# Optimization experiments

Hardware: AMD Instinct MI355X
Metric: run time of the kernel (lower is better)

## Reference

```python
import jax, jax.numpy as jnp
import numpy as np

INF = 1.0e12
B, L, D, H = 8, 128, 512, 8
DV = D // H

def _xavier(key, shape, fan_in, fan_out):
    a = float(np.sqrt(6.0 / (fan_in + fan_out)))
    return jax.random.uniform(key, shape, jnp.float32, -a, a)

def setup_inputs() -> dict:
    key = jax.random.key(0)
    ks = jax.random.split(key, 12)
    inp = jax.random.normal(ks[0], (B, L, D), jnp.float32)
    relation_inp = jax.random.normal(ks[1], (B, L, L, D), jnp.float32)
    mask = jnp.zeros((B, L, L), dtype=bool)  # no padding masked
    adj_mask = jax.random.randint(ks[2], (B, H, L, L), 0, 2).astype(jnp.int32)
    idx = jnp.arange(L)
    adj_mask = adj_mask.at[:, :, idx, idx].set(1)  # ensure non-empty neighborhoods
    rel_pos_mat = jnp.zeros((B, L, L), jnp.int32)
    deprel_mat = jnp.zeros((B, L, L), jnp.int32)
    deparc_mat = jnp.zeros((B, L, L), jnp.int32)
    W_value = _xavier(ks[3], (D, H * DV), D, H * DV)
    W_relation = _xavier(ks[4], (D, H * DV), D, H * DV)
    # weight vectors have torch shape (1,1,1,H,DV); xavier fan over last 2 dims
    w_src = _xavier(ks[5], (H, DV), H, DV)
    w_tgt = _xavier(ks[6], (H, DV), H, DV)
    w_rel = _xavier(ks[7], (H, DV), H, DV)
    W_final = _xavier(ks[8], (2 * D, D), 2 * D, D)
    b_final = jnp.zeros((D,), jnp.float32)
    return {"inp": inp, "relation_inp": relation_inp, "mask": mask,
            "adj_mask": adj_mask, "rel_pos_mat": rel_pos_mat,
            "deprel_mat": deprel_mat, "deparc_mat": deparc_mat,
            "W_value": W_value, "W_relation": W_relation,
            "w_src": w_src, "w_tgt": w_tgt, "w_rel": w_rel,
            "W_final": W_final, "b_final": b_final}

def _leaky(x):
    return jnp.where(x >= 0, x, 0.2 * x)

def reference(inp, relation_inp, mask, adj_mask, rel_pos_mat, deprel_mat,
              deparc_mat, W_value, W_relation, w_src, w_tgt, w_rel,
              W_final, b_final):
    b, l, d = inp.shape
    h, dv = w_src.shape
    # value: [B,H,L,DV]
    value = (inp @ W_value).reshape(b, l, h, dv).transpose(0, 2, 1, 3)
    # additive GAT scores without materializing [B,L,L,H,DV] src/tgt tensors
    e_src = jnp.einsum('bhld,hd->bhl', value, w_src)  # source index j
    e_tgt = jnp.einsum('bhld,hd->bhl', value, w_tgt)  # target index i
    scores_value = _leaky(e_tgt[:, :, :, None] + e_src[:, :, None, :])  # [B,H,L,L]
    # relation projection: [B,L,L,H,DV]
    relation = (relation_inp @ W_relation).reshape(b, l, l, h, dv)
    scores_relation = _leaky(jnp.einsum('bijhd,hd->bhij', relation, w_rel))
    # masks
    pad = mask[:, None]                       # [B,1,L,L] True = masked
    noadj = adj_mask == 0                     # [B,H,L,L]
    bad = pad | noadj
    scores_value = jnp.where(bad, -INF, scores_value)
    scores_relation = jnp.where(bad, -INF, scores_relation)
    attn_value = jax.nn.softmax(scores_value, axis=-1)
    attn_relation = jax.nn.softmax(scores_relation, axis=-1)
    # normalized: multiply by 1/adj (0 where no edge since adj in {0,1}), L1 renorm
    adjf = adj_mask.astype(attn_value.dtype)
    def renorm(a):
        a = a * adjf
        s = jnp.sum(jnp.abs(a), axis=-1, keepdims=True)
        return a / jnp.maximum(s, 1e-12)
    attn_value = renorm(attn_value)
    attn_relation = renorm(attn_relation)
    # zero masked / non-adjacent entries
    attn_value = jnp.where(bad, 0.0, attn_value)
    attn_relation = jnp.where(bad, 0.0, attn_relation)
    out_v = jnp.einsum('bhij,bhjd->bhid', attn_value, value)
    out_r = jnp.einsum('bhij,bhjd->bhid', attn_relation, value)
    out_v = out_v.transpose(0, 2, 1, 3).reshape(b, l, h * dv)
    out_r = out_r.transpose(0, 2, 1, 3).reshape(b, l, h * dv)
    final = jnp.concatenate([out_v, out_r], axis=-1) @ W_final + b_final
    final = final + inp
    return final, attn_value, attn_relation
```

## Files before the change

### kernel.cpp

```cpp
#include <hip/hip_runtime.h>

#define B_ 8
#define L_ 128
#define D_ 512
#define H_ 8

__device__ __forceinline__ float leaky(float v) { return fmaxf(v, 0.2f * v); }

__global__ __launch_bounds__(256) void k_value_wreff(
        const float* __restrict__ inp, const float* __restrict__ Wv,
        const float* __restrict__ wsrc, const float* __restrict__ wtgt,
        const float* __restrict__ Wrel, const float* __restrict__ wrel,
        float* __restrict__ value_t, float* __restrict__ e_src,
        float* __restrict__ e_tgt, float* __restrict__ wr_eff) {
    __shared__ float xs[4][512];
    const int t = threadIdx.x;

    if (blockIdx.x >= 256) {
        int g = (blockIdx.x - 256) * 256 + t;
        int k = g >> 3, h = g & 7;
        const float4* a = (const float4*)(Wrel + k * 512 + h * 64);
        const float4* b = (const float4*)(wrel + h * 64);
        float acc = 0.f;
#pragma unroll
        for (int q = 0; q < 16; q++) {
            float4 av = a[q], bv = b[q];
            acc += av.x * bv.x + av.y * bv.y + av.z * bv.z + av.w * bv.w;
        }
        wr_eff[k * 8 + h] = acc;
        return;
    }

    const int row0 = blockIdx.x * 4;
    {
        int r = t >> 6, seg = t & 63;
        const float4* ip = (const float4*)(inp + (size_t)(row0 + r) * 512 + seg * 8);
        float4 a = ip[0], bq = ip[1];
        *(float4*)&xs[r][seg * 8]     = a;
        *(float4*)&xs[r][seg * 8 + 4] = bq;
    }
    __syncthreads();
    const int c0 = t * 2;
    float acc[4][2] = {};
    for (int k0 = 0; k0 < 512; k0 += 4) {
        float4 xr[4];
#pragma unroll
        for (int r = 0; r < 4; r++) xr[r] = *(const float4*)&xs[r][k0];
#define VSTEP(COMP, I)                                                          \
        {                                                                       \
            float2 wv = *(const float2*)(Wv + (size_t)(k0 + I) * 512 + c0);     \
            _Pragma("unroll")                                                   \
            for (int r = 0; r < 4; r++) {                                       \
                acc[r][0] = fmaf(xr[r].COMP, wv.x, acc[r][0]);                  \
                acc[r][1] = fmaf(xr[r].COMP, wv.y, acc[r][1]);                  \
            }                                                                   \
        }
        VSTEP(x, 0) VSTEP(y, 1) VSTEP(z, 2) VSTEP(w, 3)
#undef VSTEP
    }
    const int h = t >> 5;
    const int d0 = c0 & 63;
    const int b = row0 >> 7, l0 = row0 & 127;
    {
        float4 v0 = make_float4(acc[0][0], acc[1][0], acc[2][0], acc[3][0]);
        float4 v1 = make_float4(acc[0][1], acc[1][1], acc[2][1], acc[3][1]);
        *(float4*)&value_t[((size_t)((b * 8 + h) * 64 + d0)) * 128 + l0] = v0;
        *(float4*)&value_t[((size_t)((b * 8 + h) * 64 + d0 + 1)) * 128 + l0] = v1;
    }
    float ws0 = wsrc[c0], ws1 = wsrc[c0 + 1];
    float wt0 = wtgt[c0], wt1 = wtgt[c0 + 1];
    float es[4], et[4];
#pragma unroll
    for (int r = 0; r < 4; r++) {
        es[r] = acc[r][0] * ws0 + acc[r][1] * ws1;
        et[r] = acc[r][0] * wt0 + acc[r][1] * wt1;
    }
#pragma unroll
    for (int off = 16; off >= 1; off >>= 1)
#pragma unroll
        for (int r = 0; r < 4; r++) {
            es[r] += __shfl_xor(es[r], off, 64);
            et[r] += __shfl_xor(et[r], off, 64);
        }
    if ((t & 31) == 0) {
#pragma unroll
        for (int r = 0; r < 4; r++) {
            e_src[(b * 8 + h) * 128 + l0 + r] = es[r];
            e_tgt[(b * 8 + h) * 128 + l0 + r] = et[r];
        }
    }
}

__global__ __launch_bounds__(256) void k_srel(const float* __restrict__ rel,
                                              const float* __restrict__ wr_eff,
                                              float* __restrict__ s_rel) {
    const int lane = threadIdx.x & 63;
    const int wave = (blockIdx.x * 256 + threadIdx.x) >> 6;

    float wrl[64];
    {
        const float4* wp = (const float4*)(wr_eff + lane * 64);
#pragma unroll
        for (int q = 0; q < 16; q++) {
            float4 v = wp[q];
            wrl[q * 4 + 0] = v.x; wrl[q * 4 + 1] = v.y;
            wrl[q * 4 + 2] = v.z; wrl[q * 4 + 3] = v.w;
        }
    }

    const bool hi32 = (lane & 32) != 0;
    const bool hi16 = (lane & 16) != 0;
    const bool hi8  = (lane & 8) != 0;
    const int  hsel = (lane >> 3) & 7;

#pragma unroll 2
    for (int it = 0; it < 16; ++it) {
        int row = wave + it * 8192;
        const float4* rp = (const float4*)(rel + (size_t)row * 512 + lane * 8);
        float4 u0 = rp[0];
        float4 u1 = rp[1];
        float x[8];
        x[0] = u0.x; x[1] = u0.y; x[2] = u0.z; x[3] = u0.w;
        x[4] = u1.x; x[5] = u1.y; x[6] = u1.z; x[7] = u1.w;
        float acc[8] = {0.f,0.f,0.f,0.f,0.f,0.f,0.f,0.f};
#pragma unroll
        for (int kk = 0; kk < 8; kk++)
#pragma unroll
            for (int h = 0; h < 8; h++)
                acc[h] = fmaf(x[kk], wrl[kk * 8 + h], acc[h]);

        float a4[4];
#pragma unroll
        for (int hh = 0; hh < 4; hh++) {
            float send = hi32 ? acc[hh] : acc[hh + 4];
            float recv = __shfl_xor(send, 32, 64);
            float own  = hi32 ? acc[hh + 4] : acc[hh];
            a4[hh] = own + recv;
        }
        float a2[2];
#pragma unroll
        for (int hh = 0; hh < 2; hh++) {
            float send = hi16 ? a4[hh] : a4[hh + 2];
            float recv = __shfl_xor(send, 16, 64);
            float own  = hi16 ? a4[hh + 2] : a4[hh];
            a2[hh] = own + recv;
        }
        float send = hi8 ? a2[0] : a2[1];
        float recv = __shfl_xor(send, 8, 64);
        float a1 = (hi8 ? a2[1] : a2[0]) + recv;
        a1 += __shfl_xor(a1, 4, 64);
        a1 += __shfl_xor(a1, 2, 64);
        a1 += __shfl_xor(a1, 1, 64);

        if ((lane & 7) == 0) {
            float v = leaky(a1);
            int b = row >> 14, rem = row & 16383;
            s_rel[(((size_t)(b * 8 + hsel)) << 14) + rem] = v;
        }
    }
}

__global__ __launch_bounds__(256) void k_attn(const float* s_rel,
                                              const float* __restrict__ value_t,
                                              const float* __restrict__ e_src,
                                              const float* __restrict__ e_tgt,
                                              const int* __restrict__ adj,
                                              const unsigned char* __restrict__ mask,
                                              float* __restrict__ X,
                                              float* __restrict__ out_av,
                                              float* out_ar) {
    __shared__ float lav[4][128];
    __shared__ float lar[4][128];
    const int t = threadIdx.x;
    const int bh = blockIdx.x >> 5;
    const int iq = blockIdx.x & 31;
    const int b = bh >> 3;

    const int lane = t & 63;
    const int w = t >> 6;
    const int i = iq * 4 + w;
    const size_t rowbase = ((size_t)bh * 128 + i) * 128;
    const float etg = e_tgt[bh * 128 + i];
    const int j0 = lane, j1 = lane + 64;

    float sv0 = leaky(etg + e_src[bh * 128 + j0]);
    float sv1 = leaky(etg + e_src[bh * 128 + j1]);
    float sr0 = s_rel[rowbase + j0];
    float sr1 = s_rel[rowbase + j1];
    int a0 = adj[rowbase + j0], a1 = adj[rowbase + j1];
    unsigned char m0 = mask[(size_t)(b * 128 + i) * 128 + j0];
    unsigned char m1 = mask[(size_t)(b * 128 + i) * 128 + j1];
    bool bad0 = m0 || (a0 == 0);
    bool bad1 = m1 || (a1 == 0);
    if (bad0) { sv0 = -1e30f; sr0 = -1e30f; }
    if (bad1) { sv1 = -1e30f; sr1 = -1e30f; }

    float mv = fmaxf(sv0, sv1), mr = fmaxf(sr0, sr1);
#pragma unroll
    for (int off = 32; off >= 1; off >>= 1) {
        mv = fmaxf(mv, __shfl_xor(mv, off, 64));
        mr = fmaxf(mr, __shfl_xor(mr, off, 64));
    }
    float pv0 = bad0 ? 0.f : __expf(sv0 - mv);
    float pv1 = bad1 ? 0.f : __expf(sv1 - mv);
    float pr0 = bad0 ? 0.f : __expf(sr0 - mr);
    float pr1 = bad1 ? 0.f : __expf(sr1 - mr);
    float sumv = pv0 + pv1, sumr = pr0 + pr1;
#pragma unroll
    for (int off = 32; off >= 1; off >>= 1) {
        sumv += __shfl_xor(sumv, off, 64);
        sumr += __shfl_xor(sumr, off, 64);
    }
    float iv = 1.f / fmaxf(sumv, 1e-12f);
    float ir = 1.f / fmaxf(sumr, 1e-12f);
    float av0 = pv0 * iv, av1 = pv1 * iv;
    float ar0 = pr0 * ir, ar1 = pr1 * ir;

    out_av[rowbase + j0] = av0;
    out_av[rowbase + j1] = av1;
    out_ar[rowbase + j0] = ar0;
    out_ar[rowbase + j1] = ar1;

    lav[w][j0] = av0; lav[w][j1] = av1;
    lar[w][j0] = ar0; lar[w][j1] = ar1;
    __syncthreads();

    const float4* vrow = (const float4*)(value_t + ((size_t)bh * 64 + lane) * 128);
    float accv = 0.f, accr = 0.f;
#pragma unroll 8
    for (int jb = 0; jb < 32; jb++) {
        float4 v4 = vrow[jb];
        float4 a4 = *(const float4*)&lav[w][jb * 4];
        float4 r4 = *(const float4*)&lar[w][jb * 4];
        accv = fmaf(a4.x, v4.x, accv); accv = fmaf(a4.y, v4.y, accv);
        accv = fmaf(a4.z, v4.z, accv); accv = fmaf(a4.w, v4.w, accv);
        accr = fmaf(r4.x, v4.x, accr); accr = fmaf(r4.y, v4.y, accr);
        accr = fmaf(r4.z, v4.z, accr); accr = fmaf(r4.w, v4.w, accr);
    }
    const int hh = bh & 7;
    size_t xrow = ((size_t)(b * 128 + i)) * 1024;
    X[xrow + hh * 64 + lane] = accv;
    X[xrow + 512 + hh * 64 + lane] = accr;
}

__global__ __launch_bounds__(256) void k_final(const float* __restrict__ X,
                                               const float* __restrict__ Wf,
                                               const float* __restrict__ bias,
                                               const float* __restrict__ inp,
                                               float* __restrict__ outf) {
    __shared__ float xs[4][1024];
    const int t = threadIdx.x;
    const int row0 = blockIdx.x * 4;
    {
        const float4* src = (const float4*)(X + (size_t)row0 * 1024);
        float4* dst = (float4*)xs;
#pragma unroll
        for (int q = 0; q < 4; q++) dst[q * 256 + t] = src[q * 256 + t];
    }
    __syncthreads();
    const int c0 = t * 2;
    float acc[4][2] = {};
    for (int k0 = 0; k0 < 1024; k0 += 4) {
        float4 xr[4];
#pragma unroll
        for (int r = 0; r < 4; r++) xr[r] = *(const float4*)&xs[r][k0];
#define FSTEP(COMP, I)                                                          \
        {                                                                       \
            float2 wv = *(const float2*)(Wf + (size_t)(k0 + I) * 512 + c0);     \
            _Pragma("unroll")                                                   \
            for (int r = 0; r < 4; r++) {                                       \
                acc[r][0] = fmaf(xr[r].COMP, wv.x, acc[r][0]);                  \
                acc[r][1] = fmaf(xr[r].COMP, wv.y, acc[r][1]);                  \
            }                                                                   \
        }
        FSTEP(x, 0) FSTEP(y, 1) FSTEP(z, 2) FSTEP(w, 3)
#undef FSTEP
    }
    float b0 = bias[c0], b1 = bias[c0 + 1];
#pragma unroll
    for (int r = 0; r < 4; r++) {
        size_t ro = (size_t)(row0 + r) * 512;
        float2 iv = *(const float2*)(inp + ro + c0);
        float v0 = acc[r][0] + b0 + iv.x;
        float v1 = acc[r][1] + b1 + iv.y;
        *(float2*)&outf[ro + c0] = make_float2(v0, v1);
    }
}

extern "C" void kernel_launch(void* const* d_in, const int* in_sizes, int n_in,
                              void* d_out, int out_size, void* d_ws, size_t ws_size,
                              hipStream_t stream) {
    const float* inp  = (const float*)d_in[0];
    const float* rel  = (const float*)d_in[1];
    const unsigned char* mask = (const unsigned char*)d_in[2];
    const int*   adj  = (const int*)d_in[3];
    const float* Wv   = (const float*)d_in[7];
    const float* Wr   = (const float*)d_in[8];
    const float* wsrc = (const float*)d_in[9];
    const float* wtgt = (const float*)d_in[10];
    const float* wrel = (const float*)d_in[11];
    const float* Wf   = (const float*)d_in[12];
    const float* bfin = (const float*)d_in[13];

    float* outf   = (float*)d_out;
    float* out_av = outf + (size_t)B_ * L_ * D_;
    float* out_ar = out_av + (size_t)B_ * H_ * L_ * L_;

    char* ws = (char*)d_ws;
    float* wr_eff  = (float*)(ws);
    float* value_t = (float*)(ws + 16384);
    float* e_src   = (float*)(ws + 2113536);
    float* e_tgt   = (float*)(ws + 2146304);
    float* X       = (float*)(ws + 2179072);

    k_value_wreff<<<272, 256, 0, stream>>>(inp, Wv, wsrc, wtgt, Wr, wrel,
                                           value_t, e_src, e_tgt, wr_eff);
    k_srel<<<2048, 256, 0, stream>>>(rel, wr_eff, out_ar);
    k_attn<<<2048, 256, 0, stream>>>(out_ar, value_t, e_src, e_tgt, adj, mask,
                                     X, out_av, out_ar);
    k_final<<<256, 256, 0, stream>>>(X, Wf, bfin, inp, outf);
}
```

Measured before the change: 550.5 us.

## Fuse value projection into s_rel kernel and attention into final projection

Splits the W_rel·w_rel reduction into its own small kernel. The value/e_src/e_tgt projection blocks now run as extra blocks of the relation-score kernel, so that small GEMM overlaps the large streaming pass. The attention kernel now has each block handle four query rows across all eight heads and keep the concatenated head outputs in shared memory. It then applies W_final, bias and residual in place, which removes the X workspace round trip and one launch. In exchange, the attention stage runs with far fewer blocks and loops over heads serially, which reduces parallelism and latency hiding.

```diff
diff --git a/kernel.cpp b/kernel.cpp
--- a/kernel.cpp
+++ b/kernel.cpp
@@ -7,31 +7,100 @@
 
 __device__ __forceinline__ float leaky(float v) { return fmaxf(v, 0.2f * v); }
 
-__global__ __launch_bounds__(256) void k_value_wreff(
+__global__ __launch_bounds__(256) void k_wreff(const float* __restrict__ Wrel,
+                                               const float* __restrict__ wrel,
+                                               float* __restrict__ wr_eff) {
+    int t = blockIdx.x * 256 + threadIdx.x;
+    int k = t >> 3, h = t & 7;
+    const float4* a = (const float4*)(Wrel + k * 512 + h * 64);
+    const float4* b = (const float4*)(wrel + h * 64);
+    float acc = 0.f;
+#pragma unroll
+    for (int q = 0; q < 16; q++) {
+        float4 av = a[q], bv = b[q];
+        acc += av.x * bv.x + av.y * bv.y + av.z * bv.z + av.w * bv.w;
+    }
+    wr_eff[k * 8 + h] = acc;
+}
+
+__global__ __launch_bounds__(256) void k_srel_value(
+        const float* __restrict__ rel, const float* __restrict__ wr_eff,
         const float* __restrict__ inp, const float* __restrict__ Wv,
         const float* __restrict__ wsrc, const float* __restrict__ wtgt,
-        const float* __restrict__ Wrel, const float* __restrict__ wrel,
-        float* __restrict__ value_t, float* __restrict__ e_src,
-        float* __restrict__ e_tgt, float* __restrict__ wr_eff) {
+        float* __restrict__ s_rel, float* __restrict__ value_t,
+        float* __restrict__ e_src, float* __restrict__ e_tgt) {
     __shared__ float xs[4][512];
     const int t = threadIdx.x;
 
-    if (blockIdx.x >= 256) {
-        int g = (blockIdx.x - 256) * 256 + t;
-        int k = g >> 3, h = g & 7;
-        const float4* a = (const float4*)(Wrel + k * 512 + h * 64);
-        const float4* b = (const float4*)(wrel + h * 64);
-        float acc = 0.f;
-#pragma unroll
-        for (int q = 0; q < 16; q++) {
-            float4 av = a[q], bv = b[q];
-            acc += av.x * bv.x + av.y * bv.y + av.z * bv.z + av.w * bv.w;
-        }
-        wr_eff[k * 8 + h] = acc;
+    if (blockIdx.x < 2048) {
+        const int lane = t & 63;
+        const int wave = (blockIdx.x * 256 + t) >> 6;
+
+        float wrl[64];
+        {
+            const float4* wp = (const float4*)(wr_eff + lane * 64);
+#pragma unroll
+            for (int q = 0; q < 16; q++) {
+                float4 v = wp[q];
+                wrl[q * 4 + 0] = v.x; wrl[q * 4 + 1] = v.y;
+                wrl[q * 4 + 2] = v.z; wrl[q * 4 + 3] = v.w;
+            }
+        }
+
+        const bool hi32 = (lane & 32) != 0;
+        const bool hi16 = (lane & 16) != 0;
+        const bool hi8  = (lane & 8) != 0;
+        const int  hsel = (lane >> 3) & 7;
+
+#pragma unroll 2
+        for (int it = 0; it < 16; ++it) {
+            int row = wave + it * 8192;
+            const float4* rp = (const float4*)(rel + (size_t)row * 512 + lane * 8);
+            float4 u0 = rp[0];
+            float4 u1 = rp[1];
+            float x[8];
+            x[0] = u0.x; x[1] = u0.y; x[2] = u0.z; x[3] = u0.w;
+            x[4] = u1.x; x[5] = u1.y; x[6] = u1.z; x[7] = u1.w;
+            float acc[8] = {0.f,0.f,0.f,0.f,0.f,0.f,0.f,0.f};
+#pragma unroll
+            for (int kk = 0; kk < 8; kk++)
+#pragma unroll
+                for (int h = 0; h < 8; h++)
+                    acc[h] = fmaf(x[kk], wrl[kk * 8 + h], acc[h]);
+
+            float a4[4];
+#pragma unroll
+            for (int hh = 0; hh < 4; hh++) {
+                float send = hi32 ? acc[hh] : acc[hh + 4];
+                float recv = __shfl_xor(send, 32, 64);
+                float own  = hi32 ? acc[hh + 4] : acc[hh];
+                a4[hh] = own + recv;
+            }
+            float a2[2];
+#pragma unroll
+            for (int hh = 0; hh < 2; hh++) {
+                float send = hi16 ? a4[hh] : a4[hh + 2];
+                float recv = __shfl_xor(send, 16, 64);
+                float own  = hi16 ? a4[hh + 2] : a4[hh];
+                a2[hh] = own + recv;
+            }
+            float send = hi8 ? a2[0] : a2[1];
+            float recv = __shfl_xor(send, 8, 64);
+            float a1 = (hi8 ? a2[1] : a2[0]) + recv;
+            a1 += __shfl_xor(a1, 4, 64);
+            a1 += __shfl_xor(a1, 2, 64);
+            a1 += __shfl_xor(a1, 1, 64);
+
+            if ((lane & 7) == 0) {
+                float v = leaky(a1);
+                int b = row >> 14, rem = row & 16383;
+                s_rel[(((size_t)(b * 8 + hsel)) << 14) + rem] = v;
+            }
+        }
         return;
     }
 
-    const int row0 = blockIdx.x * 4;
+    const int row0 = (blockIdx.x - 2048) * 4;
     {
         int r = t >> 6, seg = t & 63;
         const float4* ip = (const float4*)(inp + (size_t)(row0 + r) * 512 + seg * 8);
@@ -91,179 +160,94 @@
     }
 }
 
-__global__ __launch_bounds__(256) void k_srel(const float* __restrict__ rel,
-                                              const float* __restrict__ wr_eff,
-                                              float* __restrict__ s_rel) {
-    const int lane = threadIdx.x & 63;
-    const int wave = (blockIdx.x * 256 + threadIdx.x) >> 6;
-
-    float wrl[64];
-    {
-        const float4* wp = (const float4*)(wr_eff + lane * 64);
-#pragma unroll
-        for (int q = 0; q < 16; q++) {
-            float4 v = wp[q];
-            wrl[q * 4 + 0] = v.x; wrl[q * 4 + 1] = v.y;
-            wrl[q * 4 + 2] = v.z; wrl[q * 4 + 3] = v.w;
-        }
-    }
-
-    const bool hi32 = (lane & 32) != 0;
-    const bool hi16 = (lane & 16) != 0;
-    const bool hi8  = (lane & 8) != 0;
-    const int  hsel = (lane >> 3) & 7;
-
-#pragma unroll 2
-    for (int it = 0; it < 16; ++it) {
-        int row = wave + it * 8192;
-        const float4* rp = (const float4*)(rel + (size_t)row * 512 + lane * 8);
-        float4 u0 = rp[0];
-        float4 u1 = rp[1];
-        float x[8];
-        x[0] = u0.x; x[1] = u0.y; x[2] = u0.z; x[3] = u0.w;
-        x[4] = u1.x; x[5] = u1.y; x[6] = u1.z; x[7] = u1.w;
-        float acc[8] = {0.f,0.f,0.f,0.f,0.f,0.f,0.f,0.f};
-#pragma unroll
-        for (int kk = 0; kk < 8; kk++)
-#pragma unroll
-            for (int h = 0; h < 8; h++)
-                acc[h] = fmaf(x[kk], wrl[kk * 8 + h], acc[h]);
-
-        float a4[4];
-#pragma unroll
-        for (int hh = 0; hh < 4; hh++) {
-            float send = hi32 ? acc[hh] : acc[hh + 4];
-            float recv = __shfl_xor(send, 32, 64);
-            float own  = hi32 ? acc[hh + 4] : acc[hh];
-            a4[hh] = own + recv;
-        }
-        float a2[2];
-#pragma unroll
-        for (int hh = 0; hh < 2; hh++) {
-            float send = hi16 ? a4[hh] : a4[hh + 2];
-            float recv = __shfl_xor(send, 16, 64);
-            float own  = hi16 ? a4[hh + 2] : a4[hh];
-            a2[hh] = own + recv;
-        }
-        float send = hi8 ? a2[0] : a2[1];
-        float recv = __shfl_xor(send, 8, 64);
-        float a1 = (hi8 ? a2[1] : a2[0]) + recv;
-        a1 += __shfl_xor(a1, 4, 64);
-        a1 += __shfl_xor(a1, 2, 64);
-        a1 += __shfl_xor(a1, 1, 64);
-
-        if ((lane & 7) == 0) {
-            float v = leaky(a1);
-            int b = row >> 14, rem = row & 16383;
-            s_rel[(((size_t)(b * 8 + hsel)) << 14) + rem] = v;
-        }
-    }
-}
-
-__global__ __launch_bounds__(256) void k_attn(const float* s_rel,
-                                              const float* __restrict__ value_t,
-                                              const float* __restrict__ e_src,
-                                              const float* __restrict__ e_tgt,
-                                              const int* __restrict__ adj,
-                                              const unsigned char* __restrict__ mask,
-                                              float* __restrict__ X,
-                                              float* __restrict__ out_av,
-                                              float* out_ar) {
+__global__ __launch_bounds__(256) void k_attn_final(
+        const float* s_rel, const float* __restrict__ value_t,
+        const float* __restrict__ e_src, const float* __restrict__ e_tgt,
+        const int* __restrict__ adj, const unsigned char* __restrict__ mask,
+        const float* __restrict__ Wf, const float* __restrict__ bias,
+        const float* __restrict__ inp,
+        float* __restrict__ out_av, float* out_ar, float* __restrict__ outf) {
+    __shared__ float xls[4][1024];
     __shared__ float lav[4][128];
     __shared__ float lar[4][128];
     const int t = threadIdx.x;
-    const int bh = blockIdx.x >> 5;
-    const int iq = blockIdx.x & 31;
-    const int b = bh >> 3;
-
     const int lane = t & 63;
     const int w = t >> 6;
+    const int b = blockIdx.x >> 5;
+    const int iq = blockIdx.x & 31;
     const int i = iq * 4 + w;
-    const size_t rowbase = ((size_t)bh * 128 + i) * 128;
-    const float etg = e_tgt[bh * 128 + i];
     const int j0 = lane, j1 = lane + 64;
 
-    float sv0 = leaky(etg + e_src[bh * 128 + j0]);
-    float sv1 = leaky(etg + e_src[bh * 128 + j1]);
-    float sr0 = s_rel[rowbase + j0];
-    float sr1 = s_rel[rowbase + j1];
-    int a0 = adj[rowbase + j0], a1 = adj[rowbase + j1];
-    unsigned char m0 = mask[(size_t)(b * 128 + i) * 128 + j0];
-    unsigned char m1 = mask[(size_t)(b * 128 + i) * 128 + j1];
-    bool bad0 = m0 || (a0 == 0);
-    bool bad1 = m1 || (a1 == 0);
-    if (bad0) { sv0 = -1e30f; sr0 = -1e30f; }
-    if (bad1) { sv1 = -1e30f; sr1 = -1e30f; }
-
-    float mv = fmaxf(sv0, sv1), mr = fmaxf(sr0, sr1);
-#pragma unroll
-    for (int off = 32; off >= 1; off >>= 1) {
-        mv = fmaxf(mv, __shfl_xor(mv, off, 64));
-        mr = fmaxf(mr, __shfl_xor(mr, off, 64));
-    }
-    float pv0 = bad0 ? 0.f : __expf(sv0 - mv);
-    float pv1 = bad1 ? 0.f : __expf(sv1 - mv);
-    float pr0 = bad0 ? 0.f : __expf(sr0 - mr);
-    float pr1 = bad1 ? 0.f : __expf(sr1 - mr);
-    float sumv = pv0 + pv1, sumr = pr0 + pr1;
-#pragma unroll
-    for (int off = 32; off >= 1; off >>= 1) {
-        sumv += __shfl_xor(sumv, off, 64);
-        sumr += __shfl_xor(sumr, off, 64);
-    }
-    float iv = 1.f / fmaxf(sumv, 1e-12f);
-    float ir = 1.f / fmaxf(sumr, 1e-12f);
-    float av0 = pv0 * iv, av1 = pv1 * iv;
-    float ar0 = pr0 * ir, ar1 = pr1 * ir;
-
-    out_av[rowbase + j0] = av0;
-    out_av[rowbase + j1] = av1;
-    out_ar[rowbase + j0] = ar0;
-    out_ar[rowbase + j1] = ar1;
-
-    lav[w][j0] = av0; lav[w][j1] = av1;
-    lar[w][j0] = ar0; lar[w][j1] = ar1;
+    const unsigned char m0 = mask[(size_t)(b * 128 + i) * 128 + j0];
+    const unsigned char m1 = mask[(size_t)(b * 128 + i) * 128 + j1];
+
+    for (int h = 0; h < 8; h++) {
+        const int bh = b * 8 + h;
+        const size_t rowbase = ((size_t)bh * 128 + i) * 128;
+        const float etg = e_tgt[bh * 128 + i];
+
+        float sv0 = leaky(etg + e_src[bh * 128 + j0]);
+        float sv1 = leaky(etg + e_src[bh * 128 + j1]);
+        float sr0 = s_rel[rowbase + j0];
+        float sr1 = s_rel[rowbase + j1];
+        int a0 = adj[rowbase + j0], a1 = adj[rowbase + j1];
+        bool bad0 = m0 || (a0 == 0);
+        bool bad1 = m1 || (a1 == 0);
+        if (bad0) { sv0 = -1e30f; sr0 = -1e30f; }
+        if (bad1) { sv1 = -1e30f; sr1 = -1e30f; }
+
+        float mv = fmaxf(sv0, sv1), mr = fmaxf(sr0, sr1);
+#pragma unroll
+        for (int off = 32; off >= 1; off >>= 1) {
+            mv = fmaxf(mv, __shfl_xor(mv, off, 64));
+            mr = fmaxf(mr, __shfl_xor(mr, off, 64));
+        }
+        float pv0 = bad0 ? 0.f : __expf(sv0 - mv);
+        float pv1 = bad1 ? 0.f : __expf(sv1 - mv);
+        float pr0 = bad0 ? 0.f : __expf(sr0 - mr);
+        float pr1 = bad1 ? 0.f : __expf(sr1 - mr);
+        float sumv = pv0 + pv1, sumr = pr0 + pr1;
+#pragma unroll
+        for (int off = 32; off >= 1; off >>= 1) {
+            sumv += __shfl_xor(sumv, off, 64);
+            sumr += __shfl_xor(sumr, off, 64);
+        }
+        float iv = 1.f / fmaxf(sumv, 1e-12f);
+        float ir = 1.f / fmaxf(sumr, 1e-12f);
+        float av0 = pv0 * iv, av1 = pv1 * iv;
+        float ar0 = pr0 * ir, ar1 = pr1 * ir;
+
+        out_av[rowbase + j0] = av0;
+        out_av[rowbase + j1] = av1;
+        out_ar[rowbase + j0] = ar0;
+        out_ar[rowbase + j1] = ar1;
+
+        lav[w][j0] = av0; lav[w][j1] = av1;
+        lar[w][j0] = ar0; lar[w][j1] = ar1;
+
+        const float4* vrow = (const float4*)(value_t + ((size_t)bh * 64 + lane) * 128);
+        float accv = 0.f, accr = 0.f;
+#pragma unroll 8
+        for (int jb = 0; jb < 32; jb++) {
+            float4 v4 = vrow[jb];
+            float4 a4 = *(const float4*)&lav[w][jb * 4];
+            float4 r4 = *(const float4*)&lar[w][jb * 4];
+            accv = fmaf(a4.x, v4.x, accv); accv = fmaf(a4.y, v4.y, accv);
+            accv = fmaf(a4.z, v4.z, accv); accv = fmaf(a4.w, v4.w, accv);
+            accr = fmaf(r4.x, v4.x, accr); accr = fmaf(r4.y, v4.y, accr);
+            accr = fmaf(r4.z, v4.z, accr); accr = fmaf(r4.w, v4.w, accr);
+        }
+        xls[w][h * 64 + lane] = accv;
+        xls[w][512 + h * 64 + lane] = accr;
+    }
     __syncthreads();
 
-    const float4* vrow = (const float4*)(value_t + ((size_t)bh * 64 + lane) * 128);
-    float accv = 0.f, accr = 0.f;
-#pragma unroll 8
-    for (int jb = 0; jb < 32; jb++) {
-        float4 v4 = vrow[jb];
-        float4 a4 = *(const float4*)&lav[w][jb * 4];
-        float4 r4 = *(const float4*)&lar[w][jb * 4];
-        accv = fmaf(a4.x, v4.x, accv); accv = fmaf(a4.y, v4.y, accv);
-        accv = fmaf(a4.z, v4.z, accv); accv = fmaf(a4.w, v4.w, accv);
-        accr = fmaf(r4.x, v4.x, accr); accr = fmaf(r4.y, v4.y, accr);
-        accr = fmaf(r4.z, v4.z, accr); accr = fmaf(r4.w, v4.w, accr);
-    }
-    const int hh = bh & 7;
-    size_t xrow = ((size_t)(b * 128 + i)) * 1024;
-    X[xrow + hh * 64 + lane] = accv;
-    X[xrow + 512 + hh * 64 + lane] = accr;
-}
-
-__global__ __launch_bounds__(256) void k_final(const float* __restrict__ X,
-                                               const float* __restrict__ Wf,
-                                               const float* __restrict__ bias,
-                                               const float* __restrict__ inp,
-                                               float* __restrict__ outf) {
-    __shared__ float xs[4][1024];
-    const int t = threadIdx.x;
-    const int row0 = blockIdx.x * 4;
-    {
-        const float4* src = (const float4*)(X + (size_t)row0 * 1024);
-        float4* dst = (float4*)xs;
-#pragma unroll
-        for (int q = 0; q < 4; q++) dst[q * 256 + t] = src[q * 256 + t];
-    }
-    __syncthreads();
     const int c0 = t * 2;
     float acc[4][2] = {};
     for (int k0 = 0; k0 < 1024; k0 += 4) {
         float4 xr[4];
 #pragma unroll
-        for (int r = 0; r < 4; r++) xr[r] = *(const float4*)&xs[r][k0];
+        for (int r = 0; r < 4; r++) xr[r] = *(const float4*)&xls[r][k0];
 #define FSTEP(COMP, I)                                                          \
         {                                                                       \
             float2 wv = *(const float2*)(Wf + (size_t)(k0 + I) * 512 + c0);     \
@@ -276,13 +260,14 @@
         FSTEP(x, 0) FSTEP(y, 1) FSTEP(z, 2) FSTEP(w, 3)
 #undef FSTEP
     }
+    const int row0 = blockIdx.x * 4;
     float b0 = bias[c0], b1 = bias[c0 + 1];
 #pragma unroll
     for (int r = 0; r < 4; r++) {
         size_t ro = (size_t)(row0 + r) * 512;
-        float2 iv = *(const float2*)(inp + ro + c0);
-        float v0 = acc[r][0] + b0 + iv.x;
-        float v1 = acc[r][1] + b1 + iv.y;
+        float2 ivl = *(const float2*)(inp + ro + c0);
+        float v0 = acc[r][0] + b0 + ivl.x;
+        float v1 = acc[r][1] + b1 + ivl.y;
         *(float2*)&outf[ro + c0] = make_float2(v0, v1);
     }
 }
@@ -311,12 +296,10 @@
     float* value_t = (float*)(ws + 16384);
     float* e_src   = (float*)(ws + 2113536);
     float* e_tgt   = (float*)(ws + 2146304);
-    float* X       = (float*)(ws + 2179072);
-
-    k_value_wreff<<<272, 256, 0, stream>>>(inp, Wv, wsrc, wtgt, Wr, wrel,
-                                           value_t, e_src, e_tgt, wr_eff);
-    k_srel<<<2048, 256, 0, stream>>>(rel, wr_eff, out_ar);
-    k_attn<<<2048, 256, 0, stream>>>(out_ar, value_t, e_src, e_tgt, adj, mask,
-                                     X, out_av, out_ar);
-    k_final<<<256, 256, 0, stream>>>(X, Wf, bfin, inp, outf);
+
+    k_wreff<<<16, 256, 0, stream>>>(Wr, wrel, wr_eff);
+    k_srel_value<<<2304, 256, 0, stream>>>(rel, wr_eff, inp, Wv, wsrc, wtgt,
+                                           out_ar, value_t, e_src, e_tgt);
+    k_attn_final<<<256, 256, 0, stream>>>(out_ar, value_t, e_src, e_tgt, adj, mask,
+                                          Wf, bfin, inp, out_av, out_ar, outf);
 }
```

Result: faster. 536.0 us (-2.6%).
